# Kernel tuning notes

Hardware: AMD Instinct MI355X
Metric: run time of the kernel (lower is better)

The kernel has to match this reference:

```python
import jax, jax.numpy as jnp
import numpy as np

N_NODES, N_EDGES = 20000, 2000
IN_FEATS, NUM_HEADS, OUT_FEATS, EDGE_DIM = 128, 4, 32, 64
NEG_SLOPE = 0.2


def setup_inputs() -> dict:
    key = jax.random.key(0)
    ks = jax.random.split(key, 5)
    # Unique (node, edge) incidence pairs, concrete at setup time.
    rng = np.random.default_rng(0)
    flat = np.unique(rng.integers(0, N_NODES * N_EDGES, size=220000))
    src_idx = jnp.asarray(flat // N_EDGES, dtype=jnp.int32)
    edge_idx = jnp.asarray(flat % N_EDGES, dtype=jnp.int32)
    H = jnp.zeros((N_NODES, N_EDGES), jnp.float32).at[src_idx, edge_idx].set(1.0)
    feat = jax.random.normal(ks[0], (N_NODES, IN_FEATS), jnp.float32)
    edge_feat = jax.random.normal(ks[1], (N_EDGES, EDGE_DIM), jnp.float32)
    fc_w = jax.random.normal(ks[2], (IN_FEATS, NUM_HEADS * OUT_FEATS), jnp.float32) * 0.1
    attn_src = jax.random.normal(ks[3], (1, NUM_HEADS, OUT_FEATS), jnp.float32) * 0.1
    attn_edge = jax.random.normal(ks[4], (1, NUM_HEADS, EDGE_DIM), jnp.float32) * 0.1
    return {"feat": feat, "edge_feat": edge_feat, "H": H, "fc_w": fc_w,
            "attn_src": attn_src, "attn_edge": attn_edge,
            "src_idx": src_idx, "edge_idx": edge_idx}


def reference(feat, edge_feat, H, fc_w, attn_src, attn_edge, src_idx, edge_idx):
    n_nodes = feat.shape[0]
    n_edges = H.shape[1]
    # node projection -> [N, h, d]
    feat_src = (feat @ fc_w).reshape(n_nodes, NUM_HEADS, OUT_FEATS)
    # gather per incidence pair
    src_feat = feat_src[src_idx]                       # [P, h, d]
    e_src = (src_feat * attn_src).sum(-1)              # [P, h]
    e_edge = (edge_feat[edge_idx][:, None, :] * attn_edge).sum(-1)  # [P, h]
    e = jax.nn.leaky_relu(e_src + e_edge, NEG_SLOPE)   # [P, h]
    # grouped (per-hyperedge) softmax via segment ops
    max_val = jax.ops.segment_max(e, edge_idx, num_segments=n_edges)  # [E, h]
    e_exp = jnp.exp(e - max_val[edge_idx])
    sum_exp = jax.ops.segment_sum(e_exp, edge_idx, num_segments=n_edges)
    attention = e_exp / (sum_exp[edge_idx] + 1e-9)     # [P, h]
    # aggregate messages onto hyperedges
    messages = src_feat * attention[..., None]         # [P, h, d]
    hyper_edge_feats = jax.ops.segment_sum(messages, edge_idx, num_segments=n_edges)  # [E, h, d]
    # dense disseminate back to nodes
    rst = jnp.einsum('ne,ehd->nhd', H, hyper_edge_feats)
    return rst.reshape(n_nodes, NUM_HEADS * OUT_FEATS)
```

## Files before the change

### kernel.cpp

```cpp
#include <hip/hip_runtime.h>
#include <hip/hip_bf16.h>

#define N_NODES 20000
#define N_EDGES 2000
#define IN_FEATS 128
#define NUM_HEADS 4
#define OUT_FEATS 32
#define EDGE_DIM 64
#define C_FEATS 128
#define NEG_SLOPE 0.2f
#define MAXD 256
#define WT_LD 136
#define NTILES (N_NODES / 16)
#define PROJ_BLKS ((NTILES + 3) / 4)
#define K1_BLK 512
#define K1_THR 256
#define CUR_STRIDE 16

typedef __attribute__((ext_vector_type(8))) short bf16x8;
typedef __attribute__((ext_vector_type(4))) float f32x4;

__device__ __forceinline__ float leaky(float x) { return (x > 0.f) ? x : NEG_SLOPE * x; }
__device__ __forceinline__ short f2bf(float x) {
    __hip_bfloat16 h = __float2bfloat16(x);
    return *reinterpret_cast<short*>(&h);
}

__global__ __launch_bounds__(K1_THR) void proj_scatter_kernel(
    const float* __restrict__ feat, const float* __restrict__ fc_w,
    const float* __restrict__ attn_src,
    const int* __restrict__ src_idx, const int* __restrict__ edge_idx, int P,
    __hip_bfloat16* __restrict__ feat_bf, float* __restrict__ s_buf,
    int* __restrict__ cursor, int* __restrict__ node_start, int* __restrict__ edge_nodes)
{
    __shared__ unsigned short Wt[128 * WT_LD];
    const int t = threadIdx.x;
    const int bid = blockIdx.x;

    if (bid < PROJ_BLKS) {
        for (int q = t; q < 64 * 128; q += K1_THR) {
            const int c = q & 127, k = (q >> 7) * 2;
            Wt[c * WT_LD + k]     = (unsigned short)f2bf(fc_w[k * C_FEATS + c]);
            Wt[c * WT_LD + k + 1] = (unsigned short)f2bf(fc_w[(k + 1) * C_FEATS + c]);
        }
        __syncthreads();

        const int wave = t >> 6, lane = t & 63;
        const int wid = bid * 4 + wave;
        if (wid < NTILES) {
            const int m0 = wid * 16;
            const int lrow = lane & 15, lk = lane >> 4;

            bf16x8 afr[4];
            const float* arow = feat + (size_t)(m0 + lrow) * IN_FEATS + lk * 8;
            #pragma unroll
            for (int kt = 0; kt < 4; ++kt) {
                const float4 f0 = *(const float4*)(arow + kt * 32);
                const float4 f1 = *(const float4*)(arow + kt * 32 + 4);
                bf16x8 a;
                a[0] = f2bf(f0.x); a[1] = f2bf(f0.y); a[2] = f2bf(f0.z); a[3] = f2bf(f0.w);
                a[4] = f2bf(f1.x); a[5] = f2bf(f1.y); a[6] = f2bf(f1.z); a[7] = f2bf(f1.w);
                afr[kt] = a;
            }

            f32x4 acc[8];
            #pragma unroll
            for (int nt = 0; nt < 8; ++nt) acc[nt] = (f32x4){0.f, 0.f, 0.f, 0.f};
            #pragma unroll
            for (int nt = 0; nt < 8; ++nt) {
                const unsigned short* wrow = &Wt[(nt * 16 + lrow) * WT_LD + lk * 8];
                #pragma unroll
                for (int kt = 0; kt < 4; ++kt) {
                    const bf16x8 b = *(const bf16x8*)(wrow + kt * 32);
                    acc[nt] = __builtin_amdgcn_mfma_f32_16x16x32_bf16(afr[kt], b, acc[nt], 0, 0, 0);
                }
            }

            #pragma unroll
            for (int nt = 0; nt < 8; ++nt) {
                const int c = nt * 16 + lrow;
                #pragma unroll
                for (int r = 0; r < 4; ++r)
                    feat_bf[(size_t)(m0 + lk * 4 + r) * C_FEATS + c] = __float2bfloat16(acc[nt][r]);
            }
            float aw[8];
            #pragma unroll
            for (int nt = 0; nt < 8; ++nt) aw[nt] = attn_src[nt * 16 + lrow];
            #pragma unroll
            for (int h = 0; h < NUM_HEADS; ++h) {
                #pragma unroll
                for (int r = 0; r < 4; ++r) {
                    float v = acc[2 * h][r] * aw[2 * h] + acc[2 * h + 1][r] * aw[2 * h + 1];
                    v += __shfl_xor(v, 1);
                    v += __shfl_xor(v, 2);
                    v += __shfl_xor(v, 4);
                    v += __shfl_xor(v, 8);
                    if (lrow == 0) s_buf[(m0 + lk * 4 + r) * NUM_HEADS + h] = v;
                }
            }
        }
    } else {
        const int nthreads = (K1_BLK - PROJ_BLKS) * K1_THR;
        for (int p = (bid - PROJ_BLKS) * K1_THR + t; p < P; p += nthreads) {
            const int e = edge_idx[p];
            const int s = src_idx[p];
            const int pos = atomicAdd(&cursor[e * CUR_STRIDE], 1);
            if (pos < MAXD) edge_nodes[e * MAXD + pos] = s;
            const int prev = (p == 0) ? -1 : src_idx[p - 1];
            for (int n = prev + 1; n <= s; ++n) node_start[n] = p;
            if (p == P - 1)
                for (int n = s + 1; n <= N_NODES; ++n) node_start[n] = P;
        }
    }
}

__global__ __launch_bounds__(512) void edge_attn_kernel(
    const float* __restrict__ s_buf, const float* __restrict__ edge_feat,
    const float* __restrict__ attn_edge, const __hip_bfloat16* __restrict__ feat_bf,
    const int* __restrict__ cursor, const int* __restrict__ edge_nodes,
    __hip_bfloat16* __restrict__ hef)
{
    __shared__ float4 w_sh[MAXD];
    __shared__ int    n_sh[MAXD];
    __shared__ float  te_sh[NUM_HEADS];
    __shared__ float  inv_sh[NUM_HEADS];
    __shared__ float  wred[8][NUM_HEADS];
    __shared__ float  red[8][C_FEATS];

    const int e = blockIdx.x;
    const int t = threadIdx.x;
    const int wv = t >> 6, lane = t & 63;

    if (t < EDGE_DIM) {
        const float v = edge_feat[e * EDGE_DIM + t];
        #pragma unroll
        for (int h = 0; h < NUM_HEADS; ++h) {
            float p = v * attn_edge[h * EDGE_DIM + t];
            p += __shfl_xor(p, 32); p += __shfl_xor(p, 16); p += __shfl_xor(p, 8);
            p += __shfl_xor(p, 4);  p += __shfl_xor(p, 2);  p += __shfl_xor(p, 1);
            if (t == 0) te_sh[h] = p;
        }
    }
    __syncthreads();

    const int m = min(cursor[e * CUR_STRIDE], MAXD);
    const int m_pad = (m + 31) & ~31;

    float ps0 = 0.f, ps1 = 0.f, ps2 = 0.f, ps3 = 0.f;
    if (t < m) {
        const int n = edge_nodes[e * MAXD + t];
        n_sh[t] = n;
        const float4 s4 = *(const float4*)&s_buf[n * NUM_HEADS];
        float4 w;
        w.x = __expf(leaky(s4.x + te_sh[0]));
        w.y = __expf(leaky(s4.y + te_sh[1]));
        w.z = __expf(leaky(s4.z + te_sh[2]));
        w.w = __expf(leaky(s4.w + te_sh[3]));
        w_sh[t] = w;
        ps0 = w.x; ps1 = w.y; ps2 = w.z; ps3 = w.w;
    } else if (t < m_pad) {
        n_sh[t] = 0;
        w_sh[t] = make_float4(0.f, 0.f, 0.f, 0.f);
    }
    #pragma unroll
    for (int d = 32; d >= 1; d >>= 1) {
        ps0 += __shfl_xor(ps0, d); ps1 += __shfl_xor(ps1, d);
        ps2 += __shfl_xor(ps2, d); ps3 += __shfl_xor(ps3, d);
    }
    if (lane == 0) {
        wred[wv][0] = ps0; wred[wv][1] = ps1; wred[wv][2] = ps2; wred[wv][3] = ps3;
    }
    __syncthreads();
    if (t < NUM_HEADS) {
        float s = 0.f;
        #pragma unroll
        for (int w8 = 0; w8 < 8; ++w8) s += wred[w8][t];
        inv_sh[t] = 1.f / (s + 1e-9f);
    }
    __syncthreads();

    const int c0 = lane * 2;
    const int h = lane >> 4;
    float a0 = 0.f, a1 = 0.f;
    const unsigned short* fb = (const unsigned short*)feat_bf;
    #pragma unroll 8
    for (int j = wv; j < m_pad; j += 8) {
        const int n = n_sh[j];
        const float w = ((const float*)&w_sh[j])[h];
        const unsigned v = *(const unsigned*)(fb + (size_t)n * C_FEATS + c0);
        a0 += w * __uint_as_float(v << 16);
        a1 += w * __uint_as_float(v & 0xffff0000u);
    }
    red[wv][c0] = a0;
    red[wv][c0 + 1] = a1;
    __syncthreads();
    if (t < C_FEATS) {
        float r = 0.f;
        #pragma unroll
        for (int w8 = 0; w8 < 8; ++w8) r += red[w8][t];
        hef[e * C_FEATS + t] = __float2bfloat16(r * inv_sh[t >> 5]);
    }
}

#define K3_NODES 8
#define K3_CHUNK 512
__global__ __launch_bounds__(256) void disseminate_kernel(
    const int* __restrict__ node_start, const int* __restrict__ edge_idx,
    const __hip_bfloat16* __restrict__ hef, float* __restrict__ out)
{
    __shared__ int e_sh[K3_CHUNK];
    __shared__ int ns_sh[K3_NODES + 1];
    const int t = threadIdx.x;
    const int wv = t >> 6, lane = t & 63;
    const int c0 = lane * 2;
    const int n0 = blockIdx.x * K3_NODES;

    if (t < K3_NODES + 1) ns_sh[t] = node_start[n0 + t];
    __syncthreads();
    const int s0 = ns_sh[0], s1 = ns_sh[K3_NODES];

    float a00 = 0.f, a01 = 0.f, a10 = 0.f, a11 = 0.f;
    const unsigned short* hu = (const unsigned short*)hef;

    for (int cb = s0; cb < s1; cb += K3_CHUNK) {
        const int ccnt = min(K3_CHUNK, s1 - cb);
        __syncthreads();
        for (int i = t; i < ccnt; i += 256) e_sh[i] = edge_idx[cb + i];
        __syncthreads();
        {
            const int jlo = max(ns_sh[wv * 2], cb);
            const int jhi = min(ns_sh[wv * 2 + 1], cb + ccnt);
            #pragma unroll 8
            for (int j = jlo; j < jhi; ++j) {
                const unsigned v = *(const unsigned*)(hu + (size_t)e_sh[j - cb] * C_FEATS + c0);
                a00 += __uint_as_float(v << 16);
                a01 += __uint_as_float(v & 0xffff0000u);
            }
        }
        {
            const int jlo = max(ns_sh[wv * 2 + 1], cb);
            const int jhi = min(ns_sh[wv * 2 + 2], cb + ccnt);
            #pragma unroll 8
            for (int j = jlo; j < jhi; ++j) {
                const unsigned v = *(const unsigned*)(hu + (size_t)e_sh[j - cb] * C_FEATS + c0);
                a10 += __uint_as_float(v << 16);
                a11 += __uint_as_float(v & 0xffff0000u);
            }
        }
    }
    float2 r0 = make_float2(a00, a01);
    float2 r1 = make_float2(a10, a11);
    *(float2*)&out[(size_t)(n0 + wv * 2)     * C_FEATS + c0] = r0;
    *(float2*)&out[(size_t)(n0 + wv * 2 + 1) * C_FEATS + c0] = r1;
}

extern "C" void kernel_launch(void* const* d_in, const int* in_sizes, int n_in,
                              void* d_out, int out_size, void* d_ws, size_t ws_size,
                              hipStream_t stream) {
    const float* feat      = (const float*)d_in[0];
    const float* edge_feat = (const float*)d_in[1];
    const float* fc_w      = (const float*)d_in[3];
    const float* attn_src  = (const float*)d_in[4];
    const float* attn_edge = (const float*)d_in[5];
    const int*   src_idx   = (const int*)d_in[6];
    const int*   edge_idx  = (const int*)d_in[7];
    const int P = in_sizes[6];
    float* out = (float*)d_out;

    float* ws = (float*)d_ws;
    float*          s_buf      = ws;
    __hip_bfloat16* hef        = (__hip_bfloat16*)(s_buf + N_NODES * NUM_HEADS);
    __hip_bfloat16* feat_bf    = hef + N_EDGES * C_FEATS;
    int*            node_start = (int*)(feat_bf + (size_t)N_NODES * C_FEATS);
    int*            edge_nodes = node_start + (N_NODES + 1);
    int*            cursor     = edge_nodes + N_EDGES * MAXD;

    hipMemsetAsync(cursor, 0, N_EDGES * CUR_STRIDE * sizeof(int), stream);
    proj_scatter_kernel<<<K1_BLK, K1_THR, 0, stream>>>(
        feat, fc_w, attn_src, src_idx, edge_idx, P,
        feat_bf, s_buf, cursor, node_start, edge_nodes);
    edge_attn_kernel<<<N_EDGES, 512, 0, stream>>>(
        s_buf, edge_feat, attn_edge, feat_bf, cursor, edge_nodes, hef);
    disseminate_kernel<<<N_NODES / K3_NODES, 256, 0, stream>>>(
        node_start, edge_idx, hef, out);
}
```

Before: 56.42 us.

## Fuse edge attention and dissemination into one persistent kernel with grid barrier

Merges the per-hyperedge attention/aggregation kernel and the node dissemination kernel into a single persistent kernel of 1250 blocks. A software grid barrier (atomic counter with sleep polling) separates the two phases, and the phases share LDS through a union. Edge blocks shrink from 512 to 256 threads, so each block now loops over edges. The goal is to remove one kernel launch and its tail/drain gap. The cost is that forward progress relies on all 1250 blocks being co-resident, which launch_bounds occupancy of 5 is meant to ensure, and barrier spinning adds overhead.

```diff
diff --git a/kernel.cpp b/kernel.cpp
--- a/kernel.cpp
+++ b/kernel.cpp
@@ -16,14 +16,16 @@
 #define K1_BLK 512
 #define K1_THR 256
 #define CUR_STRIDE 16
+#define K23_BLK 1250
+#define K23_THR 256
 
 typedef __attribute__((ext_vector_type(8))) short bf16x8;
 typedef __attribute__((ext_vector_type(4))) float f32x4;
 
 __device__ __forceinline__ float leaky(float x) { return (x > 0.f) ? x : NEG_SLOPE * x; }
-__device__ __forceinline__ short f2bf(float x) {
+__device__ __forceinline__ unsigned short f2bf(float x) {
     __hip_bfloat16 h = __float2bfloat16(x);
-    return *reinterpret_cast<short*>(&h);
+    return *reinterpret_cast<unsigned short*>(&h);
 }
 
 __global__ __launch_bounds__(K1_THR) void proj_scatter_kernel(
@@ -40,8 +42,8 @@
     if (bid < PROJ_BLKS) {
         for (int q = t; q < 64 * 128; q += K1_THR) {
             const int c = q & 127, k = (q >> 7) * 2;
-            Wt[c * WT_LD + k]     = (unsigned short)f2bf(fc_w[k * C_FEATS + c]);
-            Wt[c * WT_LD + k + 1] = (unsigned short)f2bf(fc_w[(k + 1) * C_FEATS + c]);
+            Wt[c * WT_LD + k]     = f2bf(fc_w[k * C_FEATS + c]);
+            Wt[c * WT_LD + k + 1] = f2bf(fc_w[(k + 1) * C_FEATS + c]);
         }
         __syncthreads();
 
@@ -58,8 +60,10 @@
                 const float4 f0 = *(const float4*)(arow + kt * 32);
                 const float4 f1 = *(const float4*)(arow + kt * 32 + 4);
                 bf16x8 a;
-                a[0] = f2bf(f0.x); a[1] = f2bf(f0.y); a[2] = f2bf(f0.z); a[3] = f2bf(f0.w);
-                a[4] = f2bf(f1.x); a[5] = f2bf(f1.y); a[6] = f2bf(f1.z); a[7] = f2bf(f1.w);
+                a[0] = (short)f2bf(f0.x); a[1] = (short)f2bf(f0.y);
+                a[2] = (short)f2bf(f0.z); a[3] = (short)f2bf(f0.w);
+                a[4] = (short)f2bf(f1.x); a[5] = (short)f2bf(f1.y);
+                a[6] = (short)f2bf(f1.z); a[7] = (short)f2bf(f1.w);
                 afr[kt] = a;
             }
 
@@ -114,144 +118,158 @@
     }
 }
 
-__global__ __launch_bounds__(512) void edge_attn_kernel(
+union SharedU23 {
+    struct {
+        float4 w_sh[MAXD];
+        int    n_sh[MAXD];
+        float  te_sh[NUM_HEADS];
+        float  inv_sh[NUM_HEADS];
+        float  wred[4][NUM_HEADS];
+        float  red[4][C_FEATS];
+    } at;
+    struct {
+        int e_sh[512];
+        int ns_sh[9];
+    } ds;
+};
+
+__global__ __launch_bounds__(K23_THR, 5) void edge_node_kernel(
     const float* __restrict__ s_buf, const float* __restrict__ edge_feat,
     const float* __restrict__ attn_edge, const __hip_bfloat16* __restrict__ feat_bf,
     const int* __restrict__ cursor, const int* __restrict__ edge_nodes,
-    __hip_bfloat16* __restrict__ hef)
+    const int* __restrict__ node_start, const int* __restrict__ edge_idx,
+    unsigned* __restrict__ hef, unsigned* __restrict__ bar, float* __restrict__ out)
 {
-    __shared__ float4 w_sh[MAXD];
-    __shared__ int    n_sh[MAXD];
-    __shared__ float  te_sh[NUM_HEADS];
-    __shared__ float  inv_sh[NUM_HEADS];
-    __shared__ float  wred[8][NUM_HEADS];
-    __shared__ float  red[8][C_FEATS];
-
-    const int e = blockIdx.x;
+    __shared__ SharedU23 U;
     const int t = threadIdx.x;
+    const int bid = blockIdx.x;
     const int wv = t >> 6, lane = t & 63;
 
-    if (t < EDGE_DIM) {
-        const float v = edge_feat[e * EDGE_DIM + t];
+    for (int e = bid; e < N_EDGES; e += K23_BLK) {
+        __syncthreads();
+
+        if (t < EDGE_DIM) {
+            const float v = edge_feat[e * EDGE_DIM + t];
+            #pragma unroll
+            for (int h = 0; h < NUM_HEADS; ++h) {
+                float p = v * attn_edge[h * EDGE_DIM + t];
+                p += __shfl_xor(p, 32); p += __shfl_xor(p, 16); p += __shfl_xor(p, 8);
+                p += __shfl_xor(p, 4);  p += __shfl_xor(p, 2);  p += __shfl_xor(p, 1);
+                if (t == 0) U.at.te_sh[h] = p;
+            }
+        }
+        __syncthreads();
+
+        const int m = min(cursor[e * CUR_STRIDE], MAXD);
+        const int m_pad = (m + 31) & ~31;
+
+        float ps0 = 0.f, ps1 = 0.f, ps2 = 0.f, ps3 = 0.f;
+        if (t < m) {
+            const int n = edge_nodes[e * MAXD + t];
+            U.at.n_sh[t] = n;
+            const float4 s4 = *(const float4*)&s_buf[n * NUM_HEADS];
+            float4 w;
+            w.x = __expf(leaky(s4.x + U.at.te_sh[0]));
+            w.y = __expf(leaky(s4.y + U.at.te_sh[1]));
+            w.z = __expf(leaky(s4.z + U.at.te_sh[2]));
+            w.w = __expf(leaky(s4.w + U.at.te_sh[3]));
+            U.at.w_sh[t] = w;
+            ps0 = w.x; ps1 = w.y; ps2 = w.z; ps3 = w.w;
+        } else if (t < m_pad) {
+            U.at.n_sh[t] = 0;
+            U.at.w_sh[t] = make_float4(0.f, 0.f, 0.f, 0.f);
+        }
         #pragma unroll
-        for (int h = 0; h < NUM_HEADS; ++h) {
-            float p = v * attn_edge[h * EDGE_DIM + t];
-            p += __shfl_xor(p, 32); p += __shfl_xor(p, 16); p += __shfl_xor(p, 8);
-            p += __shfl_xor(p, 4);  p += __shfl_xor(p, 2);  p += __shfl_xor(p, 1);
-            if (t == 0) te_sh[h] = p;
-        }
+        for (int d = 32; d >= 1; d >>= 1) {
+            ps0 += __shfl_xor(ps0, d); ps1 += __shfl_xor(ps1, d);
+            ps2 += __shfl_xor(ps2, d); ps3 += __shfl_xor(ps3, d);
+        }
+        if (lane == 0) {
+            U.at.wred[wv][0] = ps0; U.at.wred[wv][1] = ps1;
+            U.at.wred[wv][2] = ps2; U.at.wred[wv][3] = ps3;
+        }
+        __syncthreads();
+        if (t < NUM_HEADS)
+            U.at.inv_sh[t] = 1.f / (U.at.wred[0][t] + U.at.wred[1][t] +
+                                    U.at.wred[2][t] + U.at.wred[3][t] + 1e-9f);
+        __syncthreads();
+
+        const int c0 = lane * 2;
+        const int h = lane >> 4;
+        float a0 = 0.f, a1 = 0.f;
+        const unsigned short* fb = (const unsigned short*)feat_bf;
+        #pragma unroll 8
+        for (int j = wv; j < m_pad; j += 4) {
+            const int n = U.at.n_sh[j];
+            const float w = ((const float*)&U.at.w_sh[j])[h];
+            const unsigned v = *(const unsigned*)(fb + (size_t)n * C_FEATS + c0);
+            a0 += w * __uint_as_float(v << 16);
+            a1 += w * __uint_as_float(v & 0xffff0000u);
+        }
+        U.at.red[wv][c0] = a0;
+        U.at.red[wv][c0 + 1] = a1;
+        __syncthreads();
+        if (t < 64) {
+            const float inv = U.at.inv_sh[t >> 4];
+            const float r0 = (U.at.red[0][2 * t]     + U.at.red[1][2 * t] +
+                              U.at.red[2][2 * t]     + U.at.red[3][2 * t]) * inv;
+            const float r1 = (U.at.red[0][2 * t + 1] + U.at.red[1][2 * t + 1] +
+                              U.at.red[2][2 * t + 1] + U.at.red[3][2 * t + 1]) * inv;
+            const unsigned u = ((unsigned)f2bf(r1) << 16) | (unsigned)f2bf(r0);
+            __hip_atomic_store(&hef[e * 64 + t], u, __ATOMIC_RELAXED, __HIP_MEMORY_SCOPE_AGENT);
+        }
+    }
+
+    asm volatile("s_waitcnt vmcnt(0)" ::: "memory");
+    __syncthreads();
+    if (t == 0) {
+        unsigned tk = __hip_atomic_fetch_add(bar, 1u, __ATOMIC_RELAXED, __HIP_MEMORY_SCOPE_AGENT);
+        unsigned goal = (tk / K23_BLK + 1u) * K23_BLK;
+        while (__hip_atomic_load(bar, __ATOMIC_RELAXED, __HIP_MEMORY_SCOPE_AGENT) < goal)
+            __builtin_amdgcn_s_sleep(8);
     }
     __syncthreads();
-
-    const int m = min(cursor[e * CUR_STRIDE], MAXD);
-    const int m_pad = (m + 31) & ~31;
-
-    float ps0 = 0.f, ps1 = 0.f, ps2 = 0.f, ps3 = 0.f;
-    if (t < m) {
-        const int n = edge_nodes[e * MAXD + t];
-        n_sh[t] = n;
-        const float4 s4 = *(const float4*)&s_buf[n * NUM_HEADS];
-        float4 w;
-        w.x = __expf(leaky(s4.x + te_sh[0]));
-        w.y = __expf(leaky(s4.y + te_sh[1]));
-        w.z = __expf(leaky(s4.z + te_sh[2]));
-        w.w = __expf(leaky(s4.w + te_sh[3]));
-        w_sh[t] = w;
-        ps0 = w.x; ps1 = w.y; ps2 = w.z; ps3 = w.w;
-    } else if (t < m_pad) {
-        n_sh[t] = 0;
-        w_sh[t] = make_float4(0.f, 0.f, 0.f, 0.f);
+    asm volatile("" ::: "memory");
+
+    for (int g = bid; g < N_NODES / 8; g += K23_BLK) {
+        __syncthreads();
+        if (t < 9) U.ds.ns_sh[t] = node_start[g * 8 + t];
+        __syncthreads();
+        const int s0 = U.ds.ns_sh[0], s1 = U.ds.ns_sh[8];
+        const int c0 = lane * 2;
+
+        float a00 = 0.f, a01 = 0.f, a10 = 0.f, a11 = 0.f;
+
+        for (int cb = s0; cb < s1; cb += 512) {
+            const int ccnt = min(512, s1 - cb);
+            __syncthreads();
+            for (int i = t; i < ccnt; i += K23_THR) U.ds.e_sh[i] = edge_idx[cb + i];
+            __syncthreads();
+            {
+                const int jlo = max(U.ds.ns_sh[wv * 2], cb);
+                const int jhi = min(U.ds.ns_sh[wv * 2 + 1], cb + ccnt);
+                #pragma unroll 8
+                for (int j = jlo; j < jhi; ++j) {
+                    const unsigned v = hef[(size_t)U.ds.e_sh[j - cb] * 64 + lane];
+                    a00 += __uint_as_float(v << 16);
+                    a01 += __uint_as_float(v & 0xffff0000u);
+                }
+            }
+            {
+                const int jlo = max(U.ds.ns_sh[wv * 2 + 1], cb);
+                const int jhi = min(U.ds.ns_sh[wv * 2 + 2], cb + ccnt);
+                #pragma unroll 8
+                for (int j = jlo; j < jhi; ++j) {
+                    const unsigned v = hef[(size_t)U.ds.e_sh[j - cb] * 64 + lane];
+                    a10 += __uint_as_float(v << 16);
+                    a11 += __uint_as_float(v & 0xffff0000u);
+                }
+            }
+        }
+        const int n0 = g * 8;
+        *(float2*)&out[(size_t)(n0 + wv * 2)     * C_FEATS + c0] = make_float2(a00, a01);
+        *(float2*)&out[(size_t)(n0 + wv * 2 + 1) * C_FEATS + c0] = make_float2(a10, a11);
     }
-    #pragma unroll
-    for (int d = 32; d >= 1; d >>= 1) {
-        ps0 += __shfl_xor(ps0, d); ps1 += __shfl_xor(ps1, d);
-        ps2 += __shfl_xor(ps2, d); ps3 += __shfl_xor(ps3, d);
-    }
-    if (lane == 0) {
-        wred[wv][0] = ps0; wred[wv][1] = ps1; wred[wv][2] = ps2; wred[wv][3] = ps3;
-    }
-    __syncthreads();
-    if (t < NUM_HEADS) {
-        float s = 0.f;
-        #pragma unroll
-        for (int w8 = 0; w8 < 8; ++w8) s += wred[w8][t];
-        inv_sh[t] = 1.f / (s + 1e-9f);
-    }
-    __syncthreads();
-
-    const int c0 = lane * 2;
-    const int h = lane >> 4;
-    float a0 = 0.f, a1 = 0.f;
-    const unsigned short* fb = (const unsigned short*)feat_bf;
-    #pragma unroll 8
-    for (int j = wv; j < m_pad; j += 8) {
-        const int n = n_sh[j];
-        const float w = ((const float*)&w_sh[j])[h];
-        const unsigned v = *(const unsigned*)(fb + (size_t)n * C_FEATS + c0);
-        a0 += w * __uint_as_float(v << 16);
-        a1 += w * __uint_as_float(v & 0xffff0000u);
-    }
-    red[wv][c0] = a0;
-    red[wv][c0 + 1] = a1;
-    __syncthreads();
-    if (t < C_FEATS) {
-        float r = 0.f;
-        #pragma unroll
-        for (int w8 = 0; w8 < 8; ++w8) r += red[w8][t];
-        hef[e * C_FEATS + t] = __float2bfloat16(r * inv_sh[t >> 5]);
-    }
-}
-
-#define K3_NODES 8
-#define K3_CHUNK 512
-__global__ __launch_bounds__(256) void disseminate_kernel(
-    const int* __restrict__ node_start, const int* __restrict__ edge_idx,
-    const __hip_bfloat16* __restrict__ hef, float* __restrict__ out)
-{
-    __shared__ int e_sh[K3_CHUNK];
-    __shared__ int ns_sh[K3_NODES + 1];
-    const int t = threadIdx.x;
-    const int wv = t >> 6, lane = t & 63;
-    const int c0 = lane * 2;
-    const int n0 = blockIdx.x * K3_NODES;
-
-    if (t < K3_NODES + 1) ns_sh[t] = node_start[n0 + t];
-    __syncthreads();
-    const int s0 = ns_sh[0], s1 = ns_sh[K3_NODES];
-
-    float a00 = 0.f, a01 = 0.f, a10 = 0.f, a11 = 0.f;
-    const unsigned short* hu = (const unsigned short*)hef;
-
-    for (int cb = s0; cb < s1; cb += K3_CHUNK) {
-        const int ccnt = min(K3_CHUNK, s1 - cb);
-        __syncthreads();
-        for (int i = t; i < ccnt; i += 256) e_sh[i] = edge_idx[cb + i];
-        __syncthreads();
-        {
-            const int jlo = max(ns_sh[wv * 2], cb);
-            const int jhi = min(ns_sh[wv * 2 + 1], cb + ccnt);
-            #pragma unroll 8
-            for (int j = jlo; j < jhi; ++j) {
-                const unsigned v = *(const unsigned*)(hu + (size_t)e_sh[j - cb] * C_FEATS + c0);
-                a00 += __uint_as_float(v << 16);
-                a01 += __uint_as_float(v & 0xffff0000u);
-            }
-        }
-        {
-            const int jlo = max(ns_sh[wv * 2 + 1], cb);
-            const int jhi = min(ns_sh[wv * 2 + 2], cb + ccnt);
-            #pragma unroll 8
-            for (int j = jlo; j < jhi; ++j) {
-                const unsigned v = *(const unsigned*)(hu + (size_t)e_sh[j - cb] * C_FEATS + c0);
-                a10 += __uint_as_float(v << 16);
-                a11 += __uint_as_float(v & 0xffff0000u);
-            }
-        }
-    }
-    float2 r0 = make_float2(a00, a01);
-    float2 r1 = make_float2(a10, a11);
-    *(float2*)&out[(size_t)(n0 + wv * 2)     * C_FEATS + c0] = r0;
-    *(float2*)&out[(size_t)(n0 + wv * 2 + 1) * C_FEATS + c0] = r1;
 }
 
 extern "C" void kernel_launch(void* const* d_in, const int* in_sizes, int n_in,
@@ -269,18 +287,18 @@
 
     float* ws = (float*)d_ws;
     float*          s_buf      = ws;
-    __hip_bfloat16* hef        = (__hip_bfloat16*)(s_buf + N_NODES * NUM_HEADS);
-    __hip_bfloat16* feat_bf    = hef + N_EDGES * C_FEATS;
+    unsigned*       hef        = (unsigned*)(s_buf + N_NODES * NUM_HEADS);
+    __hip_bfloat16* feat_bf    = (__hip_bfloat16*)(hef + N_EDGES * 64);
     int*            node_start = (int*)(feat_bf + (size_t)N_NODES * C_FEATS);
     int*            edge_nodes = node_start + (N_NODES + 1);
     int*            cursor     = edge_nodes + N_EDGES * MAXD;
-
-    hipMemsetAsync(cursor, 0, N_EDGES * CUR_STRIDE * sizeof(int), stream);
+    unsigned*       bar        = (unsigned*)(cursor + N_EDGES * CUR_STRIDE);
+
+    hipMemsetAsync(cursor, 0, (N_EDGES * CUR_STRIDE) * sizeof(int) + 64, stream);
     proj_scatter_kernel<<<K1_BLK, K1_THR, 0, stream>>>(
         feat, fc_w, attn_src, src_idx, edge_idx, P,
         feat_bf, s_buf, cursor, node_start, edge_nodes);
-    edge_attn_kernel<<<N_EDGES, 512, 0, stream>>>(
-        s_buf, edge_feat, attn_edge, feat_bf, cursor, edge_nodes, hef);
-    disseminate_kernel<<<N_NODES / K3_NODES, 256, 0, stream>>>(
-        node_start, edge_idx, hef, out);
+    edge_node_kernel<<<K23_BLK, K23_THR, 0, stream>>>(
+        s_buf, edge_feat, attn_edge, feat_bf, cursor, edge_nodes,
+        node_start, edge_idx, hef, bar, out);
 }
```

Measured after the change: 116.7 us. 2.07x slower.

## Fuse dissemination into edge attention kernel via atomic scatter to output

Applied to the files above, without the earlier changes.

Drops the separate disseminate kernel. The edge attention kernel now keeps each hyperedge's aggregated row in shared memory and atomically adds it into the output rows of that edge's member nodes. The projection kernel zeroes the output first. This removes a kernel launch and the bf16 hyperedge feature round trip, at the cost of about 220k×128 float atomics to global memory, and it makes the summation order nondeterministic.

```diff
diff --git a/kernel.cpp b/kernel.cpp
--- a/kernel.cpp
+++ b/kernel.cpp
@@ -21,9 +21,9 @@
 typedef __attribute__((ext_vector_type(4))) float f32x4;
 
 __device__ __forceinline__ float leaky(float x) { return (x > 0.f) ? x : NEG_SLOPE * x; }
-__device__ __forceinline__ short f2bf(float x) {
+__device__ __forceinline__ unsigned short f2bf(float x) {
     __hip_bfloat16 h = __float2bfloat16(x);
-    return *reinterpret_cast<short*>(&h);
+    return *reinterpret_cast<unsigned short*>(&h);
 }
 
 __global__ __launch_bounds__(K1_THR) void proj_scatter_kernel(
@@ -31,17 +31,25 @@
     const float* __restrict__ attn_src,
     const int* __restrict__ src_idx, const int* __restrict__ edge_idx, int P,
     __hip_bfloat16* __restrict__ feat_bf, float* __restrict__ s_buf,
-    int* __restrict__ cursor, int* __restrict__ node_start, int* __restrict__ edge_nodes)
+    int* __restrict__ cursor, int* __restrict__ node_start, int* __restrict__ edge_nodes,
+    float* __restrict__ out)
 {
     __shared__ unsigned short Wt[128 * WT_LD];
     const int t = threadIdx.x;
     const int bid = blockIdx.x;
 
+    {
+        const f32x4 z = {0.f, 0.f, 0.f, 0.f};
+        const size_t total4 = (size_t)N_NODES * C_FEATS / 4;
+        for (size_t i = (size_t)bid * K1_THR + t; i < total4; i += (size_t)K1_BLK * K1_THR)
+            *(f32x4*)&out[i * 4] = z;
+    }
+
     if (bid < PROJ_BLKS) {
         for (int q = t; q < 64 * 128; q += K1_THR) {
             const int c = q & 127, k = (q >> 7) * 2;
-            Wt[c * WT_LD + k]     = (unsigned short)f2bf(fc_w[k * C_FEATS + c]);
-            Wt[c * WT_LD + k + 1] = (unsigned short)f2bf(fc_w[(k + 1) * C_FEATS + c]);
+            Wt[c * WT_LD + k]     = f2bf(fc_w[k * C_FEATS + c]);
+            Wt[c * WT_LD + k + 1] = f2bf(fc_w[(k + 1) * C_FEATS + c]);
         }
         __syncthreads();
 
@@ -58,8 +66,10 @@
                 const float4 f0 = *(const float4*)(arow + kt * 32);
                 const float4 f1 = *(const float4*)(arow + kt * 32 + 4);
                 bf16x8 a;
-                a[0] = f2bf(f0.x); a[1] = f2bf(f0.y); a[2] = f2bf(f0.z); a[3] = f2bf(f0.w);
-                a[4] = f2bf(f1.x); a[5] = f2bf(f1.y); a[6] = f2bf(f1.z); a[7] = f2bf(f1.w);
+                a[0] = (short)f2bf(f0.x); a[1] = (short)f2bf(f0.y);
+                a[2] = (short)f2bf(f0.z); a[3] = (short)f2bf(f0.w);
+                a[4] = (short)f2bf(f1.x); a[5] = (short)f2bf(f1.y);
+                a[6] = (short)f2bf(f1.z); a[7] = (short)f2bf(f1.w);
                 afr[kt] = a;
             }
 
@@ -118,7 +128,7 @@
     const float* __restrict__ s_buf, const float* __restrict__ edge_feat,
     const float* __restrict__ attn_edge, const __hip_bfloat16* __restrict__ feat_bf,
     const int* __restrict__ cursor, const int* __restrict__ edge_nodes,
-    __hip_bfloat16* __restrict__ hef)
+    float* __restrict__ out)
 {
     __shared__ float4 w_sh[MAXD];
     __shared__ int    n_sh[MAXD];
@@ -126,6 +136,7 @@
     __shared__ float  inv_sh[NUM_HEADS];
     __shared__ float  wred[8][NUM_HEADS];
     __shared__ float  red[8][C_FEATS];
+    __shared__ float  row_sh[C_FEATS];
 
     const int e = blockIdx.x;
     const int t = threadIdx.x;
@@ -198,60 +209,16 @@
         float r = 0.f;
         #pragma unroll
         for (int w8 = 0; w8 < 8; ++w8) r += red[w8][t];
-        hef[e * C_FEATS + t] = __float2bfloat16(r * inv_sh[t >> 5]);
-    }
-}
-
-#define K3_NODES 8
-#define K3_CHUNK 512
-__global__ __launch_bounds__(256) void disseminate_kernel(
-    const int* __restrict__ node_start, const int* __restrict__ edge_idx,
-    const __hip_bfloat16* __restrict__ hef, float* __restrict__ out)
-{
-    __shared__ int e_sh[K3_CHUNK];
-    __shared__ int ns_sh[K3_NODES + 1];
-    const int t = threadIdx.x;
-    const int wv = t >> 6, lane = t & 63;
-    const int c0 = lane * 2;
-    const int n0 = blockIdx.x * K3_NODES;
-
-    if (t < K3_NODES + 1) ns_sh[t] = node_start[n0 + t];
-    __syncthreads();
-    const int s0 = ns_sh[0], s1 = ns_sh[K3_NODES];
-
-    float a00 = 0.f, a01 = 0.f, a10 = 0.f, a11 = 0.f;
-    const unsigned short* hu = (const unsigned short*)hef;
-
-    for (int cb = s0; cb < s1; cb += K3_CHUNK) {
-        const int ccnt = min(K3_CHUNK, s1 - cb);
-        __syncthreads();
-        for (int i = t; i < ccnt; i += 256) e_sh[i] = edge_idx[cb + i];
-        __syncthreads();
-        {
-            const int jlo = max(ns_sh[wv * 2], cb);
-            const int jhi = min(ns_sh[wv * 2 + 1], cb + ccnt);
-            #pragma unroll 8
-            for (int j = jlo; j < jhi; ++j) {
-                const unsigned v = *(const unsigned*)(hu + (size_t)e_sh[j - cb] * C_FEATS + c0);
-                a00 += __uint_as_float(v << 16);
-                a01 += __uint_as_float(v & 0xffff0000u);
-            }
-        }
-        {
-            const int jlo = max(ns_sh[wv * 2 + 1], cb);
-            const int jhi = min(ns_sh[wv * 2 + 2], cb + ccnt);
-            #pragma unroll 8
-            for (int j = jlo; j < jhi; ++j) {
-                const unsigned v = *(const unsigned*)(hu + (size_t)e_sh[j - cb] * C_FEATS + c0);
-                a10 += __uint_as_float(v << 16);
-                a11 += __uint_as_float(v & 0xffff0000u);
-            }
-        }
-    }
-    float2 r0 = make_float2(a00, a01);
-    float2 r1 = make_float2(a10, a11);
-    *(float2*)&out[(size_t)(n0 + wv * 2)     * C_FEATS + c0] = r0;
-    *(float2*)&out[(size_t)(n0 + wv * 2 + 1) * C_FEATS + c0] = r1;
+        row_sh[t] = r * inv_sh[t >> 5];
+    }
+    __syncthreads();
+
+    const int c = t & 127;
+    const int grp = t >> 7;
+    const float rc = row_sh[c];
+    for (int j = grp; j < m; j += 4) {
+        atomicAdd(&out[(size_t)n_sh[j] * C_FEATS + c], rc);
+    }
 }
 
 extern "C" void kernel_launch(void* const* d_in, const int* in_sizes, int n_in,
@@ -269,8 +236,7 @@
 
     float* ws = (float*)d_ws;
     float*          s_buf      = ws;
-    __hip_bfloat16* hef        = (__hip_bfloat16*)(s_buf + N_NODES * NUM_HEADS);
-    __hip_bfloat16* feat_bf    = hef + N_EDGES * C_FEATS;
+    __hip_bfloat16* feat_bf    = (__hip_bfloat16*)(s_buf + N_NODES * NUM_HEADS);
     int*            node_start = (int*)(feat_bf + (size_t)N_NODES * C_FEATS);
     int*            edge_nodes = node_start + (N_NODES + 1);
     int*            cursor     = edge_nodes + N_EDGES * MAXD;
@@ -278,9 +244,7 @@
     hipMemsetAsync(cursor, 0, N_EDGES * CUR_STRIDE * sizeof(int), stream);
     proj_scatter_kernel<<<K1_BLK, K1_THR, 0, stream>>>(
         feat, fc_w, attn_src, src_idx, edge_idx, P,
-        feat_bf, s_buf, cursor, node_start, edge_nodes);
+        feat_bf, s_buf, cursor, node_start, edge_nodes, out);
     edge_attn_kernel<<<N_EDGES, 512, 0, stream>>>(
-        s_buf, edge_feat, attn_edge, feat_bf, cursor, edge_nodes, hef);
-    disseminate_kernel<<<N_NODES / K3_NODES, 256, 0, stream>>>(
-        node_start, edge_idx, hef, out);
-}
+        s_buf, edge_feat, attn_edge, feat_bf, cursor, edge_nodes, out);
+}
```

After: 130.3 us. 131% more time.
